# Optimization experiments

Hardware: AMD Instinct MI355X
Metric: run time of the kernel (lower is better)

## Reference

```python
import jax, jax.numpy as jnp
import numpy as np

IN_F, OUT_F, RANK = 4096, 4096, 1024
B, S = 4, 2048


def soft_threshold24(w):
    """Soft-threshold 2:4 sparsification along the last dim.
    For each group of 4, the two smallest-magnitude entries are zeroed and the
    kept entries are shrunk by the threshold (2nd-smallest magnitude)."""
    g = w.reshape(-1, 4)
    m = jnp.abs(g)
    t = jnp.sort(m, axis=-1)[:, 1:2]  # largest pruned magnitude per group
    sp = jnp.sign(g) * jnp.maximum(m - t, 0.0)
    return sp.reshape(w.shape)


def fake_fp8_mm(a, b):
    """FP8-simulated GEMM: fp16 operands, fp32 accumulate/output (matches fake_fp8_mm)."""
    return jnp.matmul(a.astype(jnp.float16), b.astype(jnp.float16),
                      preferred_element_type=jnp.float32)


def setup_inputs() -> dict:
    key = jax.random.key(0)
    k1, k2, k3 = jax.random.split(key, 3)
    x = jax.random.normal(k1, (B, S, IN_F), dtype=jnp.float32)
    std_a = (2.0 / (IN_F + RANK)) ** 0.5   # xavier_normal for (in_features, rank)
    std_b = (2.0 / (OUT_F + RANK)) ** 0.5  # xavier_normal for (out_features, rank)
    weight_A = jax.random.normal(k2, (IN_F, RANK), dtype=jnp.float32) * std_a
    weight_B = jax.random.normal(k3, (OUT_F, RANK), dtype=jnp.float32) * std_b
    bias = jnp.zeros((OUT_F,), dtype=jnp.float32)
    scale_A = jnp.ones((), dtype=jnp.float32)  # sparse_init_scale buffer
    scale_B = jnp.ones((), dtype=jnp.float32)
    return {"x": x, "weight_A": weight_A, "weight_B": weight_B, "bias": bias,
            "scale_A": scale_A, "scale_B": scale_B}


def reference(x, weight_A, weight_B, bias, scale_A, scale_B):
    # sparse low-rank factors
    wa = soft_threshold24(weight_A) * scale_A  # (in, rank)
    wb = soft_threshold24(weight_B) * scale_B  # (out, rank)
    lead = x.shape[:-1]
    xf = x.reshape(-1, x.shape[-1])            # (T, in)
    x_proj = fake_fp8_mm(xf, wa)               # (T, rank) == x @ A_sparse
    out = fake_fp8_mm(x_proj, wb.T) + bias     # (T, out) == x_proj @ B_sparse^T + b
    return out.reshape(*lead, OUT_F)
```

## Files before the change

kernel.cpp:

```cpp
#include <hip/hip_runtime.h>

#define IN_FEAT 4096
#define OUT_FEAT 4096
#define RANK 1024
#define TOK 8192

typedef _Float16 f16x8 __attribute__((ext_vector_type(8)));
typedef _Float16 f16x4 __attribute__((ext_vector_type(4)));
typedef float f32x4 __attribute__((ext_vector_type(4)));

#define GLD_LDS16(g, l)                                                         \
  __builtin_amdgcn_global_load_lds(                                             \
      (__attribute__((address_space(1))) const void*)(g),                       \
      (__attribute__((address_space(3))) void*)(l), 16, 0, 0)

#define MIDBAR()                                        \
  __builtin_amdgcn_s_barrier();                         \
  asm volatile("s_waitcnt lgkmcnt(0)" ::: "memory")
#define ENDBAR() __builtin_amdgcn_s_barrier()


__device__ __forceinline__ void soft24(const float4 g, float s,
                                       float& r0, float& r1, float& r2, float& r3) {
  const float m0 = fabsf(g.x), m1 = fabsf(g.y), m2 = fabsf(g.z), m3 = fabsf(g.w);
  const float lo1 = fminf(m0, m1), hi1 = fmaxf(m0, m1);
  const float lo2 = fminf(m2, m3), hi2 = fmaxf(m2, m3);
  const float t = fminf(fmaxf(lo1, lo2), fminf(hi1, hi2));
  r0 = copysignf(fmaxf(m0 - t, 0.0f), g.x) * s;
  r1 = copysignf(fmaxf(m1 - t, 0.0f), g.y) * s;
  r2 = copysignf(fmaxf(m2 - t, 0.0f), g.z) * s;
  r3 = copysignf(fmaxf(m3 - t, 0.0f), g.w) * s;
}

__global__ __launch_bounds__(256) void sparsify_A_kernel(
    const float* __restrict__ wA, const float* __restrict__ scaleA,
    _Float16* __restrict__ waT) {
  const int idx = blockIdx.x * 256 + threadIdx.x;
  const int i = idx & (IN_FEAT - 1);
  const int jg = idx >> 12;
  const float4 g = *reinterpret_cast<const float4*>(wA + (size_t)i * RANK + jg * 4);
  const float s = scaleA[0];
  float r0, r1, r2, r3;
  soft24(g, s, r0, r1, r2, r3);
  const size_t base = (size_t)(jg * 4) * IN_FEAT + i;
  waT[base] = (_Float16)r0;
  waT[base + IN_FEAT] = (_Float16)r1;
  waT[base + 2 * IN_FEAT] = (_Float16)r2;
  waT[base + 3 * IN_FEAT] = (_Float16)r3;
}

__global__ __launch_bounds__(256) void sparsify_B_kernel(
    const float* __restrict__ wB, const float* __restrict__ scaleB,
    _Float16* __restrict__ wbs) {
  const int idx = blockIdx.x * 256 + threadIdx.x;
  const float4 g = *reinterpret_cast<const float4*>(wB + (size_t)idx * 4);
  const float s = scaleB[0];
  float r0, r1, r2, r3;
  soft24(g, s, r0, r1, r2, r3);
  f16x4 h;
  h[0] = (_Float16)r0; h[1] = (_Float16)r1; h[2] = (_Float16)r2; h[3] = (_Float16)r3;
  *reinterpret_cast<f16x4*>(wbs + (size_t)idx * 4) = h;
}

template <int N, int K, bool A_F32, bool OUT_F16>
__global__ __launch_bounds__(256, 4) void gemm128(
    const void* __restrict__ Av, const _Float16* __restrict__ Bh,
    void* __restrict__ Cv, const float* __restrict__ bias) {
  __shared__ __attribute__((aligned(128))) char lds[32768];
  char* ldsA = lds;
  char* ldsB = lds + 16384;

  const int tid = threadIdx.x;
  const int lane = tid & 63;
  const int w = tid >> 6;
  const int wrow = (w >> 1) * 64;
  const int wcol = (w & 1) * 64;

  constexpr int GX = N / 128;
  const int nwg = GX * (TOK / 128);
  const int l = blockIdx.y * GX + blockIdx.x;
  const int wg = (l & 7) * (nwg >> 3) + (l >> 3);
  const int brow = (wg / GX) * 128;
  const int bcol = (wg % GX) * 128;

  f32x4 acc[4][4] = {};

  for (int k0 = 0; k0 < K; k0 += 64) {
    __syncthreads();
#pragma unroll
    for (int it = 0; it < 4; ++it) {
      const int c = it * 256 + tid;
      const int row = c >> 3;
      const int u = c & 7;
      const _Float16* gsrc =
          Bh + (size_t)(bcol + row) * K + k0 + ((u ^ (row & 7)) << 3);
      GLD_LDS16(gsrc, ldsB + c * 16);
    }
    if constexpr (A_F32) {
      const float* Af = (const float*)Av;
#pragma unroll
      for (int it = 0; it < 4; ++it) {
        const int c = it * 256 + tid;
        const int row = c >> 3;
        const int u = c & 7;
        const float* gsrc = Af + (size_t)(brow + row) * K + k0 + (u << 3);
        const float4 f0 = *reinterpret_cast<const float4*>(gsrc);
        const float4 f1 = *reinterpret_cast<const float4*>(gsrc + 4);
        f16x8 h;
        h[0] = (_Float16)f0.x; h[1] = (_Float16)f0.y;
        h[2] = (_Float16)f0.z; h[3] = (_Float16)f0.w;
        h[4] = (_Float16)f1.x; h[5] = (_Float16)f1.y;
        h[6] = (_Float16)f1.z; h[7] = (_Float16)f1.w;
        *reinterpret_cast<f16x8*>(ldsA + row * 128 + ((u ^ (row & 7)) << 4)) = h;
      }
    } else {
      const _Float16* Ah = (const _Float16*)Av;
#pragma unroll
      for (int it = 0; it < 4; ++it) {
        const int c = it * 256 + tid;
        const int row = c >> 3;
        const int u = c & 7;
        const _Float16* gsrc =
            Ah + (size_t)(brow + row) * K + k0 + ((u ^ (row & 7)) << 3);
        GLD_LDS16(gsrc, ldsA + c * 16);
      }
    }
    __syncthreads();
#pragma unroll
    for (int kk = 0; kk < 2; ++kk) {
      f16x8 af[4], bf[4];
#pragma unroll
      for (int m = 0; m < 4; ++m) {
        const int row = wrow + m * 16 + (lane & 15);
        const int u = (kk * 4 + (lane >> 4)) ^ (row & 7);
        af[m] = *reinterpret_cast<const f16x8*>(ldsA + row * 128 + u * 16);
      }
#pragma unroll
      for (int n = 0; n < 4; ++n) {
        const int row = wcol + n * 16 + (lane & 15);
        const int u = (kk * 4 + (lane >> 4)) ^ (row & 7);
        bf[n] = *reinterpret_cast<const f16x8*>(ldsB + row * 128 + u * 16);
      }
#pragma unroll
      for (int m = 0; m < 4; ++m)
#pragma unroll
        for (int n = 0; n < 4; ++n)
          acc[m][n] =
              __builtin_amdgcn_mfma_f32_16x16x32_f16(af[m], bf[n], acc[m][n], 0, 0, 0);
    }
  }

  const int r4 = (lane >> 4) * 4;
  const int cl = lane & 15;
  if constexpr (OUT_F16) {
    _Float16* C = (_Float16*)Cv;
#pragma unroll
    for (int m = 0; m < 4; ++m)
#pragma unroll
      for (int n = 0; n < 4; ++n)
#pragma unroll
        for (int j = 0; j < 4; ++j) {
          const int rr = brow + wrow + m * 16 + r4 + j;
          const int cc = bcol + wcol + n * 16 + cl;
          C[(size_t)rr * N + cc] = (_Float16)acc[m][n][j];
        }
  } else {
    float* C = (float*)Cv;
#pragma unroll
    for (int n = 0; n < 4; ++n) {
      const int cc = bcol + wcol + n * 16 + cl;
      const float bv = bias[cc];
#pragma unroll
      for (int m = 0; m < 4; ++m)
#pragma unroll
        for (int j = 0; j < 4; ++j) {
          const int rr = brow + wrow + m * 16 + r4 + j;
          C[(size_t)rr * N + cc] = acc[m][n][j] + bv;
        }
    }
  }
}

template <int M, int N, int K>
__global__ __launch_bounds__(512, 2) void gemm1_f(
    const float* __restrict__ A, const _Float16* __restrict__ B,
    _Float16* __restrict__ C) {
  extern __shared__ char lds[];

  const int tid = threadIdx.x;
  const int lane = tid & 63;
  const int w = tid >> 6;
  const int wr = w >> 2;
  const int wc = w & 3;
  const int l15 = lane & 15;
  const int ubase = lane >> 4;

  constexpr int GX = N / 256;
  constexpr int NWG = GX * (M / 128);
  const int l = blockIdx.y * GX + blockIdx.x;
  const int wg = (l & 7) * (NWG >> 3) + (l >> 3);
  const int brow = (wg / GX) * 128;
  const int bcol = (wg % GX) * 256;

  f32x4 acc[4][4] = {};
  f16x8 af[4][2], bf[4][2];

  const int ar0 = tid >> 3, au0 = tid & 7;
  const int ar1 = (512 + tid) >> 3, au1 = tid & 7;
  float4 a0l, a0h, a1l, a1h;

  auto issueA = [&](int kof) {
    const float* p0 = A + (size_t)(brow + ar0) * K + kof + au0 * 8;
    const float* p1 = A + (size_t)(brow + ar1) * K + kof + au1 * 8;
    a0l = *reinterpret_cast<const float4*>(p0);
    a0h = *reinterpret_cast<const float4*>(p0 + 4);
    a1l = *reinterpret_cast<const float4*>(p1);
    a1h = *reinterpret_cast<const float4*>(p1 + 4);
  };
  auto writeA = [&](int slot) {
    f16x8 h0, h1;
    h0[0] = (_Float16)a0l.x; h0[1] = (_Float16)a0l.y;
    h0[2] = (_Float16)a0l.z; h0[3] = (_Float16)a0l.w;
    h0[4] = (_Float16)a0h.x; h0[5] = (_Float16)a0h.y;
    h0[6] = (_Float16)a0h.z; h0[7] = (_Float16)a0h.w;
    h1[0] = (_Float16)a1l.x; h1[1] = (_Float16)a1l.y;
    h1[2] = (_Float16)a1l.z; h1[3] = (_Float16)a1l.w;
    h1[4] = (_Float16)a1h.x; h1[5] = (_Float16)a1h.y;
    h1[6] = (_Float16)a1h.z; h1[7] = (_Float16)a1h.w;
    *reinterpret_cast<f16x8*>(lds + slot * 16384 + ar0 * 128 +
                              ((au0 ^ (ar0 & 7)) << 4)) = h0;
    *reinterpret_cast<f16x8*>(lds + slot * 16384 + ar1 * 128 +
                              ((au1 ^ (ar1 & 7)) << 4)) = h1;
  };
  auto stageB = [&](int kof, int slot) {
#pragma unroll
    for (int r = 0; r < 4; ++r) {
      const int c = r * 512 + tid;
      const int row = c >> 3;
      const int u = c & 7;
      GLD_LDS16(B + (size_t)(bcol + row) * K + kof + ((u ^ (row & 7)) << 3),
                lds + 49152 + slot * 32768 + c * 16);
    }
  };

  constexpr int NT = K / 64;

  issueA(0);
  stageB(0, 0);
  asm volatile("s_waitcnt vmcnt(4)" ::: "memory");
  writeA(0);
  issueA(64);
  stageB(64, 1);
  asm volatile("s_waitcnt vmcnt(8)" ::: "memory");
  asm volatile("s_waitcnt lgkmcnt(0)" ::: "memory");
  __builtin_amdgcn_s_barrier();

  int slot = 0;
  for (int t = 0; t < NT; ++t) {
#pragma unroll
    for (int i = 0; i < 4; ++i)
#pragma unroll
      for (int ks = 0; ks < 2; ++ks) {
        const int row = wr * 64 + i * 16 + l15;
        const int u = (ks * 4 + ubase) ^ (row & 7);
        af[i][ks] =
            *reinterpret_cast<const f16x8*>(lds + slot * 16384 + row * 128 + u * 16);
      }
#pragma unroll
    for (int j = 0; j < 4; ++j)
#pragma unroll
      for (int ks = 0; ks < 2; ++ks) {
        const int row = wc * 64 + j * 16 + l15;
        const int u = (ks * 4 + ubase) ^ (row & 7);
        bf[j][ks] = *reinterpret_cast<const f16x8*>(lds + 49152 + slot * 32768 +
                                                    row * 128 + u * 16);
      }
    if (t + 1 < NT) {
      int s1 = slot + 1;
      if (s1 >= 3) s1 -= 3;
      writeA(s1);
    }
    if (t + 2 < NT) {
      int s2 = slot + 2;
      if (s2 >= 3) s2 -= 3;
      issueA((t + 2) * 64);
      stageB((t + 2) * 64, s2);
      asm volatile("s_waitcnt vmcnt(8)" ::: "memory");
    } else {
      asm volatile("s_waitcnt vmcnt(0)" ::: "memory");
    }
    MIDBAR();
    __builtin_amdgcn_s_setprio(1);
#pragma unroll
    for (int ks = 0; ks < 2; ++ks)
#pragma unroll
      for (int i = 0; i < 4; ++i)
#pragma unroll
        for (int j = 0; j < 4; ++j)
          acc[i][j] = __builtin_amdgcn_mfma_f32_16x16x32_f16(
              bf[j][ks], af[i][ks], acc[i][j], 0, 0, 0);
    __builtin_amdgcn_s_setprio(0);
    ENDBAR();
    ++slot;
    if (slot == 3) slot = 0;
  }

  const int r4 = (lane >> 4) * 4;
#pragma unroll
  for (int m = 0; m < 4; ++m)
#pragma unroll
    for (int n = 0; n < 4; ++n) {
      const int rr = brow + wr * 64 + m * 16 + l15;
      const int cc = bcol + wc * 64 + n * 16 + r4;
      f16x4 h;
#pragma unroll
      for (int j = 0; j < 4; ++j) h[j] = (_Float16)acc[m][n][j];
      *reinterpret_cast<f16x4*>(C + (size_t)rr * N + cc) = h;
    }
}

#define AOFF(s, h) (((s) * 2 + (h)) * 16384)
#define BOFF(s, h) (65536 + ((s) * 2 + (h)) * 16384)

template <int M, int N, int K>
__global__ __launch_bounds__(512, 2) void gemm2_m(
    const _Float16* __restrict__ A, const _Float16* __restrict__ B,
    float* __restrict__ C, const float* __restrict__ bias) {
  extern __shared__ char lds[];

  const int tid = threadIdx.x;
  const int lane = tid & 63;
  const int w = tid >> 6;
  const int wr = w >> 2;
  const int wc = w & 3;
  const int l15 = lane & 15;
  const int ubase = lane >> 4;

  constexpr int GX = N / 256;
  constexpr int NWG = GX * (M / 256);
  const int l = blockIdx.y * GX + blockIdx.x;
  const int wg = (l & 7) * (NWG >> 3) + (l >> 3);
  const int brow = (wg / GX) * 256;
  const int bcol = (wg % GX) * 256;

  const _Float16* Abase = A + (size_t)brow * K;
  const _Float16* Bbase = B + (size_t)bcol * K;

  auto stage = [&](const _Float16* srcBase, int rowOff, int kof, int ldsOff) {
#pragma unroll
    for (int r = 0; r < 2; ++r) {
      const int c = r * 512 + tid;
      const int row = c >> 3;
      const int u = c & 7;
      const _Float16* g =
          srcBase + (size_t)(rowOff + row) * K + kof + ((u ^ (row & 7)) << 3);
      GLD_LDS16(g, lds + ldsOff + c * 16);
    }
  };

  f32x4 acc[8][4] = {};
  f16x8 af[4][2], bf01[2][2], bf23[2][2];

#define LDA_GRP(SLOT, MBASE)                                                   \
  _Pragma("unroll") for (int i = 0; i < 4; ++i)                                \
  _Pragma("unroll") for (int ks = 0; ks < 2; ++ks) {                           \
    const int row = ((MBASE) + i) * 16 + l15;                                  \
    const int u = (ks * 4 + ubase) ^ (row & 7);                                \
    af[i][ks] = *reinterpret_cast<const f16x8*>(                               \
        lds + AOFF(SLOT, wr) + row * 128 + u * 16);                            \
  }
#define LDB_GRP(SLOT, NBASE, DST)                                              \
  _Pragma("unroll") for (int j = 0; j < 2; ++j)                                \
  _Pragma("unroll") for (int ks = 0; ks < 2; ++ks) {                           \
    const int row = (wc & 1) * 64 + ((NBASE) + j) * 16 + l15;                  \
    const int u = (ks * 4 + ubase) ^ (row & 7);                                \
    DST[j][ks] = *reinterpret_cast<const f16x8*>(                              \
        lds + BOFF(SLOT, wc >> 1) + row * 128 + u * 16);                       \
  }

#define MFMA32(MO)                                                             \
  __builtin_amdgcn_s_setprio(1);                                               \
  _Pragma("unroll") for (int ks = 0; ks < 2; ++ks)                             \
  _Pragma("unroll") for (int i = 0; i < 4; ++i)                                \
  _Pragma("unroll") for (int j = 0; j < 2; ++j) {                              \
    acc[(MO) + i][j] = __builtin_amdgcn_mfma_f32_16x16x32_f16(                 \
        bf01[j][ks], af[i][ks], acc[(MO) + i][j], 0, 0, 0);                    \
    acc[(MO) + i][2 + j] = __builtin_amdgcn_mfma_f32_16x16x32_f16(             \
        bf23[j][ks], af[i][ks], acc[(MO) + i][2 + j], 0, 0, 0);                \
  }                                                                            \
  __builtin_amdgcn_s_setprio(0);

  constexpr int NT = K / 64;

  stage(Abase, 0, 0, AOFF(0, 0));
  stage(Abase, 128, 0, AOFF(0, 1));
  stage(Bbase, 0, 0, BOFF(0, 0));
  stage(Bbase, 128, 0, BOFF(0, 1));
  stage(Bbase, 0, 64, BOFF(1, 0));
  stage(Bbase, 128, 64, BOFF(1, 1));
  asm volatile("s_waitcnt vmcnt(4)" ::: "memory");
  __builtin_amdgcn_s_barrier();

  for (int tt = 0; tt < NT; tt += 2) {
    const bool last = (tt + 2 >= NT);
    const int kof1 = tt * 64 + 64;
    const int kof2 = tt * 64 + 128;
    const int kof3 = tt * 64 + 192;

    LDA_GRP(0, 0);
    LDB_GRP(0, 0, bf01);
    LDB_GRP(0, 2, bf23);
    stage(Abase, 0, kof1, AOFF(1, 0));
    stage(Abase, 128, kof1, AOFF(1, 1));
    MIDBAR();
    MFMA32(0);
    ENDBAR();

    LDA_GRP(0, 4);
    if (!last) {
      stage(Bbase, 0, kof2, BOFF(0, 0));
      stage(Bbase, 128, kof2, BOFF(0, 1));
      asm volatile("s_waitcnt vmcnt(4)" ::: "memory");
    } else {
      asm volatile("s_waitcnt vmcnt(0)" ::: "memory");
    }
    MIDBAR();
    MFMA32(4);
    ENDBAR();

    LDA_GRP(1, 0);
    LDB_GRP(1, 0, bf01);
    LDB_GRP(1, 2, bf23);
    if (!last) {
      stage(Abase, 0, kof2, AOFF(0, 0));
      stage(Abase, 128, kof2, AOFF(0, 1));
    }
    MIDBAR();
    MFMA32(0);
    ENDBAR();

    LDA_GRP(1, 4);
    if (!last) {
      stage(Bbase, 0, kof3, BOFF(1, 0));
      stage(Bbase, 128, kof3, BOFF(1, 1));
      asm volatile("s_waitcnt vmcnt(4)" ::: "memory");
    }
    MIDBAR();
    MFMA32(4);
    ENDBAR();
  }

  const int r4 = (lane >> 4) * 4;
#pragma unroll
  for (int n = 0; n < 4; ++n) {
    const int cc = bcol + wc * 64 + n * 16 + r4;
    const f32x4 bv = *reinterpret_cast<const f32x4*>(bias + cc);
#pragma unroll
    for (int m = 0; m < 8; ++m) {
      const int rr = brow + wr * 128 + m * 16 + l15;
      f32x4 o = acc[m][n] + bv;
      *reinterpret_cast<f32x4*>(C + (size_t)rr * N + cc) = o;
    }
  }
}


extern "C" void kernel_launch(void* const* d_in, const int* in_sizes, int n_in,
                              void* d_out, int out_size, void* d_ws, size_t ws_size,
                              hipStream_t stream) {
  const float* x = (const float*)d_in[0];
  const float* wA = (const float*)d_in[1];
  const float* wB = (const float*)d_in[2];
  const float* bias = (const float*)d_in[3];
  const float* scaleA = (const float*)d_in[4];
  const float* scaleB = (const float*)d_in[5];
  float* out = (float*)d_out;

  char* ws = (char*)d_ws;
  _Float16* waT = (_Float16*)ws;
  _Float16* wbs = (_Float16*)(ws + (size_t)RANK * IN_FEAT * 2);
  _Float16* xp =
      (_Float16*)(ws + (size_t)RANK * IN_FEAT * 2 + (size_t)OUT_FEAT * RANK * 2);
  const size_t needed = (size_t)RANK * IN_FEAT * 2 + (size_t)OUT_FEAT * RANK * 2 +
                        (size_t)TOK * RANK * 2;

  hipLaunchKernelGGL(sparsify_A_kernel, dim3((IN_FEAT * RANK / 4) / 256), dim3(256),
                     0, stream, wA, scaleA, waT);
  hipLaunchKernelGGL(sparsify_B_kernel, dim3((OUT_FEAT * RANK / 4) / 256), dim3(256),
                     0, stream, wB, scaleB, wbs);

  if (ws_size >= needed) {
    (void)hipFuncSetAttribute(
        reinterpret_cast<const void*>(&gemm1_f<TOK, RANK, IN_FEAT>),
        hipFuncAttributeMaxDynamicSharedMemorySize, 147456);
    hipLaunchKernelGGL((gemm1_f<TOK, RANK, IN_FEAT>),
                       dim3(RANK / 256, TOK / 128), dim3(512), 147456, stream,
                       x, waT, xp);
  } else {
    hipLaunchKernelGGL((gemm128<RANK, IN_FEAT, true, true>),
                       dim3(RANK / 128, TOK / 128), dim3(256), 0, stream,
                       (const void*)x, waT, (void*)xp, nullptr);
  }

  (void)hipFuncSetAttribute(
      reinterpret_cast<const void*>(&gemm2_m<TOK, OUT_FEAT, RANK>),
      hipFuncAttributeMaxDynamicSharedMemorySize, 131072);
  hipLaunchKernelGGL((gemm2_m<TOK, OUT_FEAT, RANK>),
                     dim3(OUT_FEAT / 256, TOK / 256), dim3(512), 131072, stream,
                     xp, wbs, out, bias);
}
```

Measured before the change: 194.3 us.

## Restructure gemm1 to 128x128 tiles with double-buffered LDS and register prefetch

Replaces the 512-thread 128x256 gemm1 kernel, which used a 3-slot dynamic LDS ring, with a 256-thread 128x128 kernel using 64KB of static LDS. It double-buffers both operands and keeps two register sets of fp32 A prefetch, loading two k-steps ahead. The in-loop barriers drop from two per k-step to one. This aims to raise occupancy and cut LDS and synchronisation overhead, at the cost of more register pressure and less B reuse per tile.

```diff
diff --git a/kernel.cpp b/kernel.cpp
--- a/kernel.cpp
+++ b/kernel.cpp
@@ -182,128 +182,144 @@
 }
 
 template <int M, int N, int K>
-__global__ __launch_bounds__(512, 2) void gemm1_f(
+__global__ __launch_bounds__(256, 2) void gemm1_h(
     const float* __restrict__ A, const _Float16* __restrict__ B,
     _Float16* __restrict__ C) {
-  extern __shared__ char lds[];
+  __shared__ __attribute__((aligned(128))) char lds[65536];
 
   const int tid = threadIdx.x;
   const int lane = tid & 63;
   const int w = tid >> 6;
-  const int wr = w >> 2;
-  const int wc = w & 3;
+  const int wr = w >> 1;
+  const int wc = w & 1;
   const int l15 = lane & 15;
   const int ubase = lane >> 4;
 
-  constexpr int GX = N / 256;
+  constexpr int GX = N / 128;
   constexpr int NWG = GX * (M / 128);
   const int l = blockIdx.y * GX + blockIdx.x;
   const int wg = (l & 7) * (NWG >> 3) + (l >> 3);
   const int brow = (wg / GX) * 128;
-  const int bcol = (wg % GX) * 256;
+  const int bcol = (wg % GX) * 128;
 
   f32x4 acc[4][4] = {};
   f16x8 af[4][2], bf[4][2];
-
-  const int ar0 = tid >> 3, au0 = tid & 7;
-  const int ar1 = (512 + tid) >> 3, au1 = tid & 7;
-  float4 a0l, a0h, a1l, a1h;
-
-  auto issueA = [&](int kof) {
-    const float* p0 = A + (size_t)(brow + ar0) * K + kof + au0 * 8;
-    const float* p1 = A + (size_t)(brow + ar1) * K + kof + au1 * 8;
-    a0l = *reinterpret_cast<const float4*>(p0);
-    a0h = *reinterpret_cast<const float4*>(p0 + 4);
-    a1l = *reinterpret_cast<const float4*>(p1);
-    a1h = *reinterpret_cast<const float4*>(p1 + 4);
-  };
-  auto writeA = [&](int slot) {
-    f16x8 h0, h1;
-    h0[0] = (_Float16)a0l.x; h0[1] = (_Float16)a0l.y;
-    h0[2] = (_Float16)a0l.z; h0[3] = (_Float16)a0l.w;
-    h0[4] = (_Float16)a0h.x; h0[5] = (_Float16)a0h.y;
-    h0[6] = (_Float16)a0h.z; h0[7] = (_Float16)a0h.w;
-    h1[0] = (_Float16)a1l.x; h1[1] = (_Float16)a1l.y;
-    h1[2] = (_Float16)a1l.z; h1[3] = (_Float16)a1l.w;
-    h1[4] = (_Float16)a1h.x; h1[5] = (_Float16)a1h.y;
-    h1[6] = (_Float16)a1h.z; h1[7] = (_Float16)a1h.w;
-    *reinterpret_cast<f16x8*>(lds + slot * 16384 + ar0 * 128 +
-                              ((au0 ^ (ar0 & 7)) << 4)) = h0;
-    *reinterpret_cast<f16x8*>(lds + slot * 16384 + ar1 * 128 +
-                              ((au1 ^ (ar1 & 7)) << 4)) = h1;
+  float4 ar0[4][2], ar1[4][2];
+
+  const int srow = tid >> 3;
+  const int su = tid & 7;
+
+  auto loadA0 = [&](int kof) {
+#pragma unroll
+    for (int r = 0; r < 4; ++r) {
+      const int row = (r * 256 + tid) >> 3;
+      const float* p = A + (size_t)(brow + row) * K + kof + su * 8;
+      ar0[r][0] = *reinterpret_cast<const float4*>(p);
+      ar0[r][1] = *reinterpret_cast<const float4*>(p + 4);
+    }
+  };
+  auto loadA1 = [&](int kof) {
+#pragma unroll
+    for (int r = 0; r < 4; ++r) {
+      const int row = (r * 256 + tid) >> 3;
+      const float* p = A + (size_t)(brow + row) * K + kof + su * 8;
+      ar1[r][0] = *reinterpret_cast<const float4*>(p);
+      ar1[r][1] = *reinterpret_cast<const float4*>(p + 4);
+    }
+  };
+  auto writeA0 = [&](int slot) {
+#pragma unroll
+    for (int r = 0; r < 4; ++r) {
+      const int row = (r * 256 + tid) >> 3;
+      f16x8 h;
+      h[0] = (_Float16)ar0[r][0].x; h[1] = (_Float16)ar0[r][0].y;
+      h[2] = (_Float16)ar0[r][0].z; h[3] = (_Float16)ar0[r][0].w;
+      h[4] = (_Float16)ar0[r][1].x; h[5] = (_Float16)ar0[r][1].y;
+      h[6] = (_Float16)ar0[r][1].z; h[7] = (_Float16)ar0[r][1].w;
+      *reinterpret_cast<f16x8*>(lds + slot * 16384 + row * 128 +
+                                ((su ^ (row & 7)) << 4)) = h;
+    }
+  };
+  auto writeA1 = [&](int slot) {
+#pragma unroll
+    for (int r = 0; r < 4; ++r) {
+      const int row = (r * 256 + tid) >> 3;
+      f16x8 h;
+      h[0] = (_Float16)ar1[r][0].x; h[1] = (_Float16)ar1[r][0].y;
+      h[2] = (_Float16)ar1[r][0].z; h[3] = (_Float16)ar1[r][0].w;
+      h[4] = (_Float16)ar1[r][1].x; h[5] = (_Float16)ar1[r][1].y;
+      h[6] = (_Float16)ar1[r][1].z; h[7] = (_Float16)ar1[r][1].w;
+      *reinterpret_cast<f16x8*>(lds + slot * 16384 + row * 128 +
+                                ((su ^ (row & 7)) << 4)) = h;
+    }
   };
   auto stageB = [&](int kof, int slot) {
 #pragma unroll
     for (int r = 0; r < 4; ++r) {
-      const int c = r * 512 + tid;
-      const int row = c >> 3;
-      const int u = c & 7;
+      const int c = r * 256 + tid;
+      const int row = c >> 3, u = c & 7;
       GLD_LDS16(B + (size_t)(bcol + row) * K + kof + ((u ^ (row & 7)) << 3),
-                lds + 49152 + slot * 32768 + c * 16);
-    }
+                lds + 32768 + slot * 16384 + c * 16);
+    }
+  };
+  auto ldfrag = [&](int p) {
+#pragma unroll
+    for (int i = 0; i < 4; ++i)
+#pragma unroll
+      for (int ks = 0; ks < 2; ++ks) {
+        const int ra = wr * 64 + i * 16 + l15;
+        const int ua = (ks * 4 + ubase) ^ (ra & 7);
+        af[i][ks] =
+            *reinterpret_cast<const f16x8*>(lds + p * 16384 + ra * 128 + ua * 16);
+        const int rb = wc * 64 + i * 16 + l15;
+        const int ub = (ks * 4 + ubase) ^ (rb & 7);
+        bf[i][ks] = *reinterpret_cast<const f16x8*>(lds + 32768 + p * 16384 +
+                                                    rb * 128 + ub * 16);
+      }
   };
 
   constexpr int NT = K / 64;
 
-  issueA(0);
+#define MFMA_BLOCK()                                                           \
+  asm volatile("s_waitcnt lgkmcnt(0)" ::: "memory");                           \
+  __builtin_amdgcn_sched_barrier(0);                                           \
+  __builtin_amdgcn_s_setprio(1);                                               \
+  _Pragma("unroll") for (int ks = 0; ks < 2; ++ks)                             \
+  _Pragma("unroll") for (int i = 0; i < 4; ++i)                                \
+  _Pragma("unroll") for (int j = 0; j < 4; ++j)                                \
+      acc[i][j] = __builtin_amdgcn_mfma_f32_16x16x32_f16(                      \
+          bf[j][ks], af[i][ks], acc[i][j], 0, 0, 0);                           \
+  __builtin_amdgcn_s_setprio(0);
+
+  loadA0(0);
   stageB(0, 0);
-  asm volatile("s_waitcnt vmcnt(4)" ::: "memory");
-  writeA(0);
-  issueA(64);
-  stageB(64, 1);
+  loadA1(64);
+  writeA0(0);
+  asm volatile("s_waitcnt lgkmcnt(0)" ::: "memory");
   asm volatile("s_waitcnt vmcnt(8)" ::: "memory");
-  asm volatile("s_waitcnt lgkmcnt(0)" ::: "memory");
   __builtin_amdgcn_s_barrier();
 
-  int slot = 0;
   for (int t = 0; t < NT; ++t) {
-#pragma unroll
-    for (int i = 0; i < 4; ++i)
-#pragma unroll
-      for (int ks = 0; ks < 2; ++ks) {
-        const int row = wr * 64 + i * 16 + l15;
-        const int u = (ks * 4 + ubase) ^ (row & 7);
-        af[i][ks] =
-            *reinterpret_cast<const f16x8*>(lds + slot * 16384 + row * 128 + u * 16);
-      }
-#pragma unroll
-    for (int j = 0; j < 4; ++j)
-#pragma unroll
-      for (int ks = 0; ks < 2; ++ks) {
-        const int row = wc * 64 + j * 16 + l15;
-        const int u = (ks * 4 + ubase) ^ (row & 7);
-        bf[j][ks] = *reinterpret_cast<const f16x8*>(lds + 49152 + slot * 32768 +
-                                                    row * 128 + u * 16);
-      }
+    const int p = t & 1;
+    ldfrag(p);
+    if (t + 1 < NT) stageB((t + 1) * 64, p ^ 1);
+    if (t + 2 < NT) {
+      if (p == 0) loadA0((t + 2) * 64);
+      else        loadA1((t + 2) * 64);
+    }
     if (t + 1 < NT) {
-      int s1 = slot + 1;
-      if (s1 >= 3) s1 -= 3;
-      writeA(s1);
-    }
+      if (p == 0) writeA1(p ^ 1);
+      else        writeA0(p ^ 1);
+    }
+    MFMA_BLOCK();
     if (t + 2 < NT) {
-      int s2 = slot + 2;
-      if (s2 >= 3) s2 -= 3;
-      issueA((t + 2) * 64);
-      stageB((t + 2) * 64, s2);
       asm volatile("s_waitcnt vmcnt(8)" ::: "memory");
     } else {
       asm volatile("s_waitcnt vmcnt(0)" ::: "memory");
     }
-    MIDBAR();
-    __builtin_amdgcn_s_setprio(1);
-#pragma unroll
-    for (int ks = 0; ks < 2; ++ks)
-#pragma unroll
-      for (int i = 0; i < 4; ++i)
-#pragma unroll
-        for (int j = 0; j < 4; ++j)
-          acc[i][j] = __builtin_amdgcn_mfma_f32_16x16x32_f16(
-              bf[j][ks], af[i][ks], acc[i][j], 0, 0, 0);
-    __builtin_amdgcn_s_setprio(0);
-    ENDBAR();
-    ++slot;
-    if (slot == 3) slot = 0;
-  }
+    __builtin_amdgcn_s_barrier();
+  }
+#undef MFMA_BLOCK
 
   const int r4 = (lane >> 4) * 4;
 #pragma unroll
@@ -490,11 +506,8 @@
                      0, stream, wB, scaleB, wbs);
 
   if (ws_size >= needed) {
-    (void)hipFuncSetAttribute(
-        reinterpret_cast<const void*>(&gemm1_f<TOK, RANK, IN_FEAT>),
-        hipFuncAttributeMaxDynamicSharedMemorySize, 147456);
-    hipLaunchKernelGGL((gemm1_f<TOK, RANK, IN_FEAT>),
-                       dim3(RANK / 256, TOK / 128), dim3(512), 147456, stream,
+    hipLaunchKernelGGL((gemm1_h<TOK, RANK, IN_FEAT>),
+                       dim3(RANK / 128, TOK / 128), dim3(256), 0, stream,
                        x, waT, xp);
   } else {
     hipLaunchKernelGGL((gemm128<RANK, IN_FEAT, true, true>),
```

New measurement: 339.8 us. 74.9% more time.
